# Kernel optimization log

Measured on AMD Instinct MI355X. Metric: run time of the kernel, lower is better.

The kernel has to match this reference:

```python
import jax, jax.numpy as jnp
import numpy as np

KNN = 8
T = 0.07
EPS = 1e-7

def l2norm(x):
    return x / jnp.sqrt(jnp.sum(x * x, axis=1, keepdims=True))

def nce_softmax_loss(x):
    # CrossEntropyLoss with all labels == 0
    return jnp.mean(jax.nn.logsumexp(x, axis=1) - x[:, 0])

def knn_indices(logits, k):
    # cos_distance_softmax on a single 'sample' [N, C]
    soft = jax.nn.softmax(logits, axis=-1)                      # [N, C]
    w = jnp.linalg.norm(soft, axis=-1)                          # [N]
    sim = (soft @ soft.T) / jnp.clip(w[:, None] * w[None, :], EPS)
    dist = 1.0 - sim
    eye = jnp.eye(logits.shape[0], dtype=dist.dtype)
    dist = dist * (1.0 - eye) - eye                             # diag -> -1 so self is always picked
    _, nbr = jax.lax.top_k(-dist, k)                            # k smallest distances
    return nbr                                                   # [N, k]

def gnn_encode(h, nbr, W, b):
    # DGL TAGConv with k=1 on the knn graph. Edges are j->i for j in knn(i),
    # so every node has in-degree KNN and D^-1/2 A D^-1/2 h == mean over knn neighbors.
    agg = jnp.mean(h[nbr], axis=1)                              # [N, C]
    return l2norm(jnp.concatenate([h, agg], axis=1) @ W + b)

def setup_inputs():
    key = jax.random.key(0)
    ks = jax.random.split(key, 16)
    B, S_DIM, T_DIM, C, N_DATA, K, NCLS = 256, 1024, 2048, 128, 200000, 4096, 100
    stdv = 1.0 / np.sqrt(C / 3.0)
    return {
        "epoch": 1,
        "f_s": jax.random.normal(ks[0], (B, S_DIM), jnp.float32),
        "l_s": jax.random.normal(ks[1], (B, NCLS), jnp.float32),
        "f_t": jax.random.normal(ks[2], (B, T_DIM), jnp.float32),
        "l_t": jax.random.normal(ks[3], (B, NCLS), jnp.float32),
        "idx": jax.random.randint(ks[4], (B,), 0, N_DATA, jnp.int32),
        "contrast_idx": jax.random.randint(ks[5], (B, K), 0, N_DATA, jnp.int32),
        "W_es": jax.random.normal(ks[6], (C, S_DIM), jnp.float32) / np.sqrt(S_DIM),
        "b_es": jnp.zeros((C,), jnp.float32),
        "W_et": jax.random.normal(ks[7], (C, T_DIM), jnp.float32) / np.sqrt(T_DIM),
        "b_et": jnp.zeros((C,), jnp.float32),
        "W_gs": jax.random.normal(ks[8], (2 * C, C), jnp.float32) / np.sqrt(2 * C),
        "b_gs": jnp.zeros((C,), jnp.float32),
        "W_gt": jax.random.normal(ks[9], (2 * C, C), jnp.float32) / np.sqrt(2 * C),
        "b_gt": jnp.zeros((C,), jnp.float32),
        "memory_l": jax.random.uniform(ks[10], (N_DATA, C), jnp.float32, -stdv, stdv),
        "memory_ab": jax.random.uniform(ks[11], (N_DATA, C), jnp.float32, -stdv, stdv),
    }

def reference(epoch, f_s, l_s, f_t, l_t, idx, contrast_idx,
              W_es, b_es, W_et, b_et, W_gs, b_gs, W_gt, b_gt,
              memory_l, memory_ab):
    mem_l = jax.lax.stop_gradient(memory_l)
    mem_ab = jax.lax.stop_gradient(memory_ab)

    # Embed + L2 normalize
    f_es = l2norm(f_s @ W_es.T + b_es)                          # [B, C]
    f_et = l2norm(f_t @ W_et.T + b_et)                          # [B, C]

    # NCEAverage.forward: gather negatives from memory banks
    weight_t = mem_l[contrast_idx]                              # [B, K, C]
    weight_s = mem_ab[contrast_idx]                             # [B, K, C]
    # get_pos
    f_us = mem_l[idx]                                           # [B, C]
    f_ut = mem_ab[idx]                                          # [B, C]

    ls_pos = jnp.sum(f_ut * f_es, axis=1, keepdims=True)        # [B, 1]
    lt_pos = jnp.sum(f_us * f_et, axis=1, keepdims=True)
    ls_neg = jnp.einsum('bkc,bc->bk', weight_t, f_es)           # [B, K]
    lt_neg = jnp.einsum('bkc,bc->bk', weight_s, f_et)
    out_s = jnp.concatenate([ls_pos, ls_neg], axis=1) / T
    out_t = jnp.concatenate([lt_pos, lt_neg], axis=1) / T
    loss = nce_softmax_loss(out_s) + nce_softmax_loss(out_t)

    # GNN branch (batchSize >= knn)
    nbr_s = knn_indices(jax.lax.stop_gradient(l_s), KNN)
    f_gs = gnn_encode(f_es, nbr_s, W_gs, b_gs)                  # [B, C]
    nbr_t = knn_indices(jax.lax.stop_gradient(l_t), KNN)
    f_gt = gnn_encode(f_et, nbr_t, W_gt, b_gt)

    # get_smooth (fully detached, momentum 0.75)
    f_sgs = jax.lax.stop_gradient(l2norm(mem_l[idx] * 0.75 + f_gs * 0.25))
    f_sgt = jax.lax.stop_gradient(l2norm(mem_ab[idx] * 0.75 + f_gt * 0.25))

    gs_pos = jnp.sum(f_sgt * f_gs, axis=1, keepdims=True)
    gt_pos = jnp.sum(f_sgs * f_gt, axis=1, keepdims=True)
    gs_neg = jnp.einsum('bkc,bc->bk', weight_t, f_gs)
    gt_neg = jnp.einsum('bkc,bc->bk', weight_s, f_gt)
    out_gs = jnp.concatenate([gs_pos, gs_neg], axis=1) / T
    out_gt = jnp.concatenate([gt_pos, gt_neg], axis=1) / T
    loss_g = nce_softmax_loss(out_gs) + nce_softmax_loss(out_gt)

    # NOTE: contrast.update() is a no-grad buffer mutation with no effect on the
    # returned loss; omitted from the pure-functional reference.
    return loss + loss_g
```

## Files before the change

### kernel.cpp

```cpp
#include <hip/hip_runtime.h>
#include <math.h>

#define B 256
#define SDIM 1024
#define TDIM 2048
#define C 128
#define NCLS 100
#define KNEG 4096
#define KNN_K 8
#define NCHUNK 16
#define KC (KNEG / NCHUNK)
#define TINV (1.0f / 0.07f)

template <int CTRL>
__device__ __forceinline__ float dpp_add(float v) {
  const int x = __builtin_amdgcn_update_dpp(0, __float_as_int(v), CTRL, 0xF, 0xF, true);
  return v + __int_as_float(x);
}
__device__ __forceinline__ float sum16(float v) {
  v = dpp_add<0xB1>(v);
  v = dpp_add<0x4E>(v);
  v = dpp_add<0x141>(v);
  v = dpp_add<0x140>(v);
  return v;
}
__device__ __forceinline__ float wave_sum64(float v) {
  v = sum16(v);
  v += __shfl_xor(v, 16, 64);
  v += __shfl_xor(v, 32, 64);
  return v;
}
__device__ __forceinline__ float dot4(float4 a, float4 b) {
  return a.x * b.x + a.y * b.y + a.z * b.z + a.w * b.w;
}

__global__ __launch_bounds__(256) void embed2_kernel(
    const float* __restrict__ Xs, const float* __restrict__ Ws,
    const float* __restrict__ bs, const float* __restrict__ Xt,
    const float* __restrict__ Wt, const float* __restrict__ bt,
    float* __restrict__ out_s, float* __restrict__ out_t) {
  const int which = blockIdx.y;
  const int S = which ? TDIM : SDIM;
  const float* __restrict__ X = which ? Xt : Xs;
  const float* __restrict__ W = which ? Wt : Ws;
  const float* __restrict__ bias = which ? bt : bs;
  float* __restrict__ out = which ? out_t : out_s;

  __shared__ float xrow[4 * TDIM];
  __shared__ float ob[4][C];
  const int b4 = blockIdx.x * 4;
  const int t = threadIdx.x;
  const int wave = t >> 6, lane = t & 63;

  const float4* xg = (const float4*)(X + (size_t)b4 * S);
  for (int i = t; i < S; i += 256) ((float4*)xrow)[i] = xg[i];
  __syncthreads();

  const int nj = S / 256;
  const int sq = S / 4;
  for (int ci = 0; ci < 32; ++ci) {
    const int c = wave * 32 + ci;
    const float4* wrow = (const float4*)(W + (size_t)c * S);
    float a0 = 0.f, a1 = 0.f, a2 = 0.f, a3 = 0.f;
    for (int j = 0; j < nj; ++j) {
      const float4 w4 = wrow[lane + 64 * j];
      a0 += dot4(w4, ((const float4*)xrow)[0 * sq + lane + 64 * j]);
      a1 += dot4(w4, ((const float4*)xrow)[1 * sq + lane + 64 * j]);
      a2 += dot4(w4, ((const float4*)xrow)[2 * sq + lane + 64 * j]);
      a3 += dot4(w4, ((const float4*)xrow)[3 * sq + lane + 64 * j]);
    }
    a0 = wave_sum64(a0); a1 = wave_sum64(a1);
    a2 = wave_sum64(a2); a3 = wave_sum64(a3);
    if (lane == 0) {
      const float bb = bias[c];
      ob[0][c] = a0 + bb; ob[1][c] = a1 + bb;
      ob[2][c] = a2 + bb; ob[3][c] = a3 + bb;
    }
  }
  __syncthreads();

  const float v1 = ob[wave][lane];
  const float v2 = ob[wave][lane + 64];
  const float ss = wave_sum64(v1 * v1 + v2 * v2);
  const float inv = 1.0f / sqrtf(ss);
  out[(size_t)(b4 + wave) * C + lane] = v1 * inv;
  out[(size_t)(b4 + wave) * C + lane + 64] = v2 * inv;
}

__global__ __launch_bounds__(128) void knn_soft_kernel(
    const float* __restrict__ Ls, const float* __restrict__ Lt,
    float* __restrict__ soft_s, float* __restrict__ soft_t,
    float* __restrict__ wn_s, float* __restrict__ wn_t) {
  const int which = blockIdx.y;
  const float* L = which ? Lt : Ls;
  float* soft = which ? soft_t : soft_s;
  float* wn = which ? wn_t : wn_s;
  const int b = blockIdx.x;
  const int t = threadIdx.x;
  const int wave = t >> 6, lane = t & 63;
  __shared__ float r2[2];

  const float x = (t < NCLS) ? L[b * NCLS + t] : -INFINITY;
  float m = x;
#pragma unroll
  for (int off = 32; off; off >>= 1) m = fmaxf(m, __shfl_xor(m, off, 64));
  if (lane == 0) r2[wave] = m;
  __syncthreads();
  m = fmaxf(r2[0], r2[1]);
  __syncthreads();

  const float e = (t < NCLS) ? expf(x - m) : 0.f;
  float s = e;
#pragma unroll
  for (int off = 32; off; off >>= 1) s += __shfl_xor(s, off, 64);
  if (lane == 0) r2[wave] = s;
  __syncthreads();
  s = r2[0] + r2[1];
  __syncthreads();

  const float p = e / s;
  if (t < NCLS) soft[b * NCLS + t] = p;

  float q = p * p;
#pragma unroll
  for (int off = 32; off; off >>= 1) q += __shfl_xor(q, off, 64);
  if (lane == 0) r2[wave] = q;
  __syncthreads();
  if (t == 0) wn[b] = sqrtf(r2[0] + r2[1]);
}

__global__ __launch_bounds__(256) void knn_topk_kernel(
    const float* __restrict__ soft_s, const float* __restrict__ wn_s,
    int* __restrict__ nbr_s, const float* __restrict__ soft_t,
    const float* __restrict__ wn_t, int* __restrict__ nbr_t) {
  const int which = blockIdx.y;
  const float* __restrict__ soft = which ? soft_t : soft_s;
  const float* __restrict__ wn = which ? wn_t : wn_s;
  int* __restrict__ nbr = which ? nbr_t : nbr_s;

  const int i = blockIdx.x;
  const int j = threadIdx.x;
  __shared__ float si[NCLS];
  __shared__ float vals[B];

  if (j < NCLS) si[j] = soft[i * NCLS + j];
  __syncthreads();

  float dot = 0.f;
  const float4* sj4 = (const float4*)(soft + j * NCLS);
#pragma unroll
  for (int c = 0; c < NCLS / 4; ++c) dot += dot4(((const float4*)si)[c], sj4[c]);
  const float denom = fmaxf(wn[i] * wn[j], 1e-7f);
  vals[j] = (j == i) ? 1.0f : (dot / denom - 1.0f);
  __syncthreads();

  if (j < 64) {
    float v0 = vals[j], v1 = vals[j + 64], v2 = vals[j + 128], v3 = vals[j + 192];
    for (int r = 0; r < KNN_K; ++r) {
      float bv = v0; int bi = j;
      if (v1 > bv) { bv = v1; bi = j + 64; }
      if (v2 > bv) { bv = v2; bi = j + 128; }
      if (v3 > bv) { bv = v3; bi = j + 192; }
#pragma unroll
      for (int off = 1; off < 64; off <<= 1) {
        const float ov = __shfl_xor(bv, off, 64);
        const int oi = __shfl_xor(bi, off, 64);
        if (ov > bv || (ov == bv && oi < bi)) { bv = ov; bi = oi; }
      }
      if (j == 0) nbr[i * KNN_K + r] = bi;
      if (j == (bi & 63)) {
        const int q = bi >> 6;
        if (q == 0) v0 = -INFINITY;
        else if (q == 1) v1 = -INFINITY;
        else if (q == 2) v2 = -INFINITY;
        else v3 = -INFINITY;
      }
    }
  }
}

__global__ __launch_bounds__(256) void gnn_pos_kernel(
    const float* __restrict__ f_es, const float* __restrict__ f_et,
    const int* __restrict__ nbr_s, const int* __restrict__ nbr_t,
    const float* __restrict__ W_gs, const float* __restrict__ b_gs,
    const float* __restrict__ W_gt, const float* __restrict__ b_gt,
    const float* __restrict__ mem_l, const float* __restrict__ mem_ab,
    const int* __restrict__ idx, float* __restrict__ f_gs_out,
    float* __restrict__ f_gt_out, float* __restrict__ pos) {
  const int b = blockIdx.x;
  const int t = threadIdx.x;
  const int half = t >> 7;
  const int c = t & 127;
  const int wave = t >> 6, lane = t & 63;

  const float* __restrict__ h = half ? f_et : f_es;
  const int* __restrict__ nbr = half ? nbr_t : nbr_s;
  const float* __restrict__ Wg = half ? W_gt : W_gs;
  const float* __restrict__ bg = half ? b_gt : b_gs;

  __shared__ float hcat[2][2 * C];
  __shared__ float gbuf[2][C];
  __shared__ float red[4];
  __shared__ float r26[2][6];

  float agg = 0.f;
#pragma unroll
  for (int j = 0; j < KNN_K; ++j)
    agg += h[(size_t)nbr[b * KNN_K + j] * C + c];
  hcat[half][c] = h[(size_t)b * C + c];
  hcat[half][C + c] = agg * (1.0f / KNN_K);
  __syncthreads();

  float acc = bg[c];
  for (int k = 0; k < 2 * C; ++k) acc += hcat[half][k] * Wg[k * C + c];

  float ss = acc * acc;
#pragma unroll
  for (int off = 32; off; off >>= 1) ss += __shfl_xor(ss, off, 64);
  if (lane == 0) red[wave] = ss;
  __syncthreads();
  const float g = acc / sqrtf(red[half * 2] + red[half * 2 + 1]);
  gbuf[half][c] = g;
  (half ? f_gt_out : f_gs_out)[(size_t)b * C + c] = g;
  __syncthreads();

  if (half == 0) {
    const int id = idx[b];
    const float ml = mem_l[(size_t)id * C + c];
    const float mab = mem_ab[(size_t)id * C + c];
    const float es = f_es[(size_t)b * C + c];
    const float et = f_et[(size_t)b * C + c];
    const float gs = gbuf[0][c];
    const float gt = gbuf[1][c];
    const float sgs = 0.75f * ml + 0.25f * gs;
    const float sgt = 0.75f * mab + 0.25f * gt;

    float v6[6] = {sgs * sgs, sgt * sgt, mab * es, ml * et, sgt * gs, sgs * gt};
#pragma unroll
    for (int q = 0; q < 6; ++q) {
      float v = v6[q];
#pragma unroll
      for (int off = 32; off; off >>= 1) v += __shfl_xor(v, off, 64);
      if (lane == 0) r26[wave][q] = v;
    }
  }
  __syncthreads();
  if (t == 0) {
    const float ss_gs = r26[0][0] + r26[1][0];
    const float ss_gt = r26[0][1] + r26[1][1];
    pos[0 * B + b] = r26[0][2] + r26[1][2];
    pos[1 * B + b] = r26[0][3] + r26[1][3];
    pos[2 * B + b] = (r26[0][4] + r26[1][4]) / sqrtf(ss_gt);
    pos[3 * B + b] = (r26[0][5] + r26[1][5]) / sqrtf(ss_gs);
  }
}

__global__ __launch_bounds__(256) void neg_partial_kernel(
    const float* __restrict__ mem_l, const float* __restrict__ mem_ab,
    const int* __restrict__ cidx, const float* __restrict__ f_es,
    const float* __restrict__ f_et, const float* __restrict__ f_gs,
    const float* __restrict__ f_gt, float* __restrict__ partial) {
  const int b = blockIdx.x;
  const int chunk = blockIdx.y;
  const int bank = blockIdx.z;
  const float* __restrict__ mem = bank ? mem_ab : mem_l;
  const float* __restrict__ f1 = bank ? f_et : f_es;
  const float* __restrict__ f2 = bank ? f_gt : f_gs;
  const int t = threadIdx.x;
  const int wave = t >> 6, lane = t & 63;
  const int grp = t >> 4;
  const int lig = t & 15;

  __shared__ int rows[KC];
  __shared__ float rbuf[4][2];

  rows[t] = cidx[(size_t)b * KNEG + chunk * KC + t];

  const float4 x1lo = ((const float4*)f1)[b * 32 + lig];
  const float4 x1hi = ((const float4*)f1)[b * 32 + lig + 16];
  const float4 x2lo = ((const float4*)f2)[b * 32 + lig];
  const float4 x2hi = ((const float4*)f2)[b * 32 + lig + 16];
  __syncthreads();

  const float4* pa = (const float4*)(mem + ((size_t)rows[grp * 16 + 0] << 7));
  const float4* pb = (const float4*)(mem + ((size_t)rows[grp * 16 + 1] << 7));
  float4 alo = pa[lig], ahi = pa[lig + 16];
  float4 blo = pb[lig], bhi = pb[lig + 16];

  float s1 = 0.f, s2 = 0.f;
  for (int it = 0; it < 16; it += 2) {
    const float4 calo = alo, cahi = ahi, cblo = blo, cbhi = bhi;
    if (it + 2 < 16) {
      const float4* na = (const float4*)(mem + ((size_t)rows[grp * 16 + it + 2] << 7));
      const float4* nb = (const float4*)(mem + ((size_t)rows[grp * 16 + it + 3] << 7));
      alo = na[lig]; ahi = na[lig + 16];
      blo = nb[lig]; bhi = nb[lig + 16];
    }
    float d1a = dot4(calo, x1lo) + dot4(cahi, x1hi);
    float d2a = dot4(calo, x2lo) + dot4(cahi, x2hi);
    float d1b = dot4(cblo, x1lo) + dot4(cbhi, x1hi);
    float d2b = dot4(cblo, x2lo) + dot4(cbhi, x2hi);
    d1a = sum16(d1a); d2a = sum16(d2a);
    d1b = sum16(d1b); d2b = sum16(d2b);
    s1 += __expf(d1a * TINV) + __expf(d1b * TINV);
    s2 += __expf(d2a * TINV) + __expf(d2b * TINV);
  }
  s1 += __shfl_xor(s1, 32, 64);
  s1 += __shfl_xor(s1, 16, 64);
  s2 += __shfl_xor(s2, 32, 64);
  s2 += __shfl_xor(s2, 16, 64);
  if (lane == 0) { rbuf[wave][0] = s1; rbuf[wave][1] = s2; }
  __syncthreads();
  if (t == 0) {
    const float v1 = rbuf[0][0] + rbuf[1][0] + rbuf[2][0] + rbuf[3][0];
    const float v2 = rbuf[0][1] + rbuf[1][1] + rbuf[2][1] + rbuf[3][1];
    partial[((size_t)bank * B + b) * NCHUNK + chunk] = v1;
    partial[((size_t)(bank + 2) * B + b) * NCHUNK + chunk] = v2;
  }
}

__global__ __launch_bounds__(256) void loss_kernel(
    const float* __restrict__ partial, const float* __restrict__ pos,
    float* __restrict__ out) {
  const int b = threadIdx.x;
  const int wave = b >> 6, lane = b & 63;
  __shared__ float rb[4];
  float contrib = 0.f;
#pragma unroll
  for (int l = 0; l < 4; ++l) {
    const float p = pos[l * B + b] * TINV;
    float s = expf(p);
    for (int ch = 0; ch < NCHUNK; ++ch)
      s += partial[((size_t)l * B + b) * NCHUNK + ch];
    contrib += logf(s) - p;
  }
#pragma unroll
  for (int off = 32; off; off >>= 1) contrib += __shfl_xor(contrib, off, 64);
  if (lane == 0) rb[wave] = contrib;
  __syncthreads();
  if (b == 0) out[0] = (rb[0] + rb[1] + rb[2] + rb[3]) * (1.0f / B);
}

extern "C" void kernel_launch(void* const* d_in, const int* in_sizes, int n_in,
                              void* d_out, int out_size, void* d_ws,
                              size_t ws_size, hipStream_t stream) {
  const float* f_s = (const float*)d_in[1];
  const float* l_s = (const float*)d_in[2];
  const float* f_t = (const float*)d_in[3];
  const float* l_t = (const float*)d_in[4];
  const int* idx = (const int*)d_in[5];
  const int* cidx = (const int*)d_in[6];
  const float* W_es = (const float*)d_in[7];
  const float* b_es = (const float*)d_in[8];
  const float* W_et = (const float*)d_in[9];
  const float* b_et = (const float*)d_in[10];
  const float* W_gs = (const float*)d_in[11];
  const float* b_gs = (const float*)d_in[12];
  const float* W_gt = (const float*)d_in[13];
  const float* b_gt = (const float*)d_in[14];
  const float* mem_l = (const float*)d_in[15];
  const float* mem_ab = (const float*)d_in[16];

  char* w = (char*)d_ws;
  float* ws_f_es = (float*)w;    w += B * C * sizeof(float);
  float* ws_f_et = (float*)w;    w += B * C * sizeof(float);
  float* ws_f_gs = (float*)w;    w += B * C * sizeof(float);
  float* ws_f_gt = (float*)w;    w += B * C * sizeof(float);
  float* ws_soft_s = (float*)w;  w += B * NCLS * sizeof(float);
  float* ws_soft_t = (float*)w;  w += B * NCLS * sizeof(float);
  float* ws_wn_s = (float*)w;    w += B * sizeof(float);
  float* ws_wn_t = (float*)w;    w += B * sizeof(float);
  int* ws_nbr_s = (int*)w;       w += B * KNN_K * sizeof(int);
  int* ws_nbr_t = (int*)w;       w += B * KNN_K * sizeof(int);
  float* ws_pos = (float*)w;     w += 4 * B * sizeof(float);
  float* ws_partial = (float*)w; w += 4 * B * NCHUNK * sizeof(float);

  embed2_kernel<<<dim3(B / 4, 2), 256, 0, stream>>>(f_s, W_es, b_es, f_t, W_et,
                                                    b_et, ws_f_es, ws_f_et);

  knn_soft_kernel<<<dim3(B, 2), 128, 0, stream>>>(l_s, l_t, ws_soft_s,
                                                  ws_soft_t, ws_wn_s, ws_wn_t);

  knn_topk_kernel<<<dim3(B, 2), 256, 0, stream>>>(ws_soft_s, ws_wn_s, ws_nbr_s,
                                                  ws_soft_t, ws_wn_t, ws_nbr_t);

  gnn_pos_kernel<<<B, 256, 0, stream>>>(ws_f_es, ws_f_et, ws_nbr_s, ws_nbr_t,
                                        W_gs, b_gs, W_gt, b_gt, mem_l, mem_ab,
                                        idx, ws_f_gs, ws_f_gt, ws_pos);

  neg_partial_kernel<<<dim3(B, NCHUNK, 2), 256, 0, stream>>>(
      mem_l, mem_ab, cidx, ws_f_es, ws_f_et, ws_f_gs, ws_f_gt, ws_partial);

  loss_kernel<<<1, 256, 0, stream>>>(ws_partial, ws_pos, (float*)d_out);
}
```

Baseline: 420.2 us.

## Sort contrast indices per row before the negative-sample gather

Adds a per-row bitonic sort kernel in shared memory that orders each row's 4096 contrast indices by memory-bank row. The negative-dot kernel then gathers rows in ascending address order. The intent is better DRAM and cache locality for the random gathers from the 200k-row memory banks. In exchange it adds a full extra kernel with many barrier-separated sort stages, plus a 4 MB workspace that is written and then read back.

Result: no change. 424.3 us (+1.0%).

```diff
diff --git a/kernel.cpp b/kernel.cpp
--- a/kernel.cpp
+++ b/kernel.cpp
@@ -32,6 +32,35 @@
 }
 __device__ __forceinline__ float dot4(float4 a, float4 b) {
   return a.x * b.x + a.y * b.y + a.z * b.z + a.w * b.w;
+}
+
+__global__ __launch_bounds__(1024) void sort_refs_kernel(
+    const int* __restrict__ cidx, int* __restrict__ sorted_rows) {
+  __shared__ unsigned key[KNEG];
+  const int b = blockIdx.x;
+  const int t = threadIdx.x;
+
+  for (int i = t; i < KNEG; i += 1024)
+    key[i] = ((unsigned)cidx[(size_t)b * KNEG + i] << 12) | (unsigned)i;
+  __syncthreads();
+
+  for (int k2 = 2; k2 <= KNEG; k2 <<= 1) {
+    for (int j = k2 >> 1; j > 0; j >>= 1) {
+#pragma unroll
+      for (int s = 0; s < KNEG / 1024; ++s) {
+        const int i = s * 1024 + t;
+        const int ixj = i ^ j;
+        if (ixj > i) {
+          const bool up = ((i & k2) == 0);
+          const unsigned a = key[i], c = key[ixj];
+          if ((a > c) == up) { key[i] = c; key[ixj] = a; }
+        }
+      }
+      __syncthreads();
+    }
+  }
+  for (int i = t; i < KNEG; i += 1024)
+    sorted_rows[(size_t)b * KNEG + i] = (int)(key[i] >> 12);
 }
 
 __global__ __launch_bounds__(256) void embed2_kernel(
@@ -257,7 +286,7 @@
 
 __global__ __launch_bounds__(256) void neg_partial_kernel(
     const float* __restrict__ mem_l, const float* __restrict__ mem_ab,
-    const int* __restrict__ cidx, const float* __restrict__ f_es,
+    const int* __restrict__ srows, const float* __restrict__ f_es,
     const float* __restrict__ f_et, const float* __restrict__ f_gs,
     const float* __restrict__ f_gt, float* __restrict__ partial) {
   const int b = blockIdx.x;
@@ -274,7 +303,7 @@
   __shared__ int rows[KC];
   __shared__ float rbuf[4][2];
 
-  rows[t] = cidx[(size_t)b * KNEG + chunk * KC + t];
+  rows[t] = srows[(size_t)b * KNEG + chunk * KC + t];
 
   const float4 x1lo = ((const float4*)f1)[b * 32 + lig];
   const float4 x1hi = ((const float4*)f1)[b * 32 + lig + 16];
@@ -374,6 +403,9 @@
   int* ws_nbr_t = (int*)w;       w += B * KNN_K * sizeof(int);
   float* ws_pos = (float*)w;     w += 4 * B * sizeof(float);
   float* ws_partial = (float*)w; w += 4 * B * NCHUNK * sizeof(float);
+  int* ws_sorted = (int*)w;      w += (size_t)B * KNEG * sizeof(int);
+
+  sort_refs_kernel<<<B, 1024, 0, stream>>>(cidx, ws_sorted);
 
   embed2_kernel<<<dim3(B / 4, 2), 256, 0, stream>>>(f_s, W_es, b_es, f_t, W_et,
                                                     b_et, ws_f_es, ws_f_et);
@@ -389,7 +421,7 @@
                                         idx, ws_f_gs, ws_f_gt, ws_pos);
 
   neg_partial_kernel<<<dim3(B, NCHUNK, 2), 256, 0, stream>>>(
-      mem_l, mem_ab, cidx, ws_f_es, ws_f_et, ws_f_gs, ws_f_gt, ws_partial);
+      mem_l, mem_ab, ws_sorted, ws_f_es, ws_f_et, ws_f_gs, ws_f_gt, ws_partial);
 
   loss_kernel<<<1, 256, 0, stream>>>(ws_partial, ws_pos, (float*)d_out);
 }
```
